# Performance work log

Hardware: AMD Instinct MI355X
Metric: run time of the kernel (lower is better)

The kernel has to match this reference:

```python
import jax, jax.numpy as jnp
import numpy as np

KAPPA = 0.5


def setup_inputs() -> dict:
    key = jax.random.key(0)
    embeddings = jax.random.normal(key, (8, 4096, 64), dtype=jnp.float32)
    return {"embeddings": embeddings}


def reference(embeddings):
    # logits[b, n, m] = kappa * <emb[b,n], emb[b,m]>   -> [B, N, N]
    logits = KAPPA * jnp.einsum("bnd,bmd->bnm", embeddings, embeddings)
    B = logits.shape[0]
    # logsumexp over both matrix dims, per batch element
    loss = jax.scipy.special.logsumexp(logits.reshape(B, -1), axis=1)
    return loss.mean()
```

## Files before the change

kernel.cpp:

```cpp
#include <hip/hip_runtime.h>
#include <math.h>

#define BATCH 8
#define NTOK  4096
#define DIM   64
#define BM    128
#define NT    (NTOK / BM)
#define TPB   (NT * (NT + 1) / 2)
#define TOTAL (BATCH * TPB)
#define GRIDP 1024
#define KAPPA 0.5f
#define LOG2E 1.4426950408889634f
#define LN2   0.6931471805599453f
#define M2FIX 48.0f

typedef _Float16 f16x8 __attribute__((ext_vector_type(8)));
typedef float    f32x16 __attribute__((ext_vector_type(16)));

__device__ __forceinline__ float EXP2(float x) {
#if __has_builtin(__builtin_amdgcn_exp2f)
    return __builtin_amdgcn_exp2f(x);
#else
    return __expf(x * LN2);
#endif
}

__global__ __launch_bounds__(256)
void conv_f16(const float* __restrict__ emb, f16x8* __restrict__ o16) {
    const size_t i = (size_t)blockIdx.x * 256 + threadIdx.x;
    const float4 v0 = *(const float4*)(emb + i * 8);
    const float4 v1 = *(const float4*)(emb + i * 8 + 4);
    f16x8 p;
    p[0] = (_Float16)v0.x; p[1] = (_Float16)v0.y;
    p[2] = (_Float16)v0.z; p[3] = (_Float16)v0.w;
    p[4] = (_Float16)v1.x; p[5] = (_Float16)v1.y;
    p[6] = (_Float16)v1.z; p[7] = (_Float16)v1.w;
    o16[i] = p;
}

__device__ __forceinline__ void decode_unit(int u, int& b, int& ti, int& tj) {
    b = u / TPB;
    int t = u - b * TPB;
    int i = 0;
    while (t >= NT - i) { t -= NT - i; ++i; }
    ti = i; tj = i + t;
}

__global__ __launch_bounds__(256, 4)
void gram_lse_partial(const f16x8* __restrict__ w16, float* __restrict__ ws) {
    __shared__ f16x8 S[2048];

    const int tid  = threadIdx.x;
    const int lane = tid & 63;
    const int w    = tid >> 6;
    const int half = lane >> 5;
    const int ln31 = lane & 31;
    const int waveR = (w & 1) * 64;
    const int waveC = (w >> 1) * 64;
    const float c2 = KAPPA * LOG2E;

    auto stage = [&](int b, int ti, int tj) {
        const char* pA16 = (const char*)(w16 + ((size_t)b * NTOK + (size_t)ti * BM) * 8);
        const char* pB16 = (const char*)(w16 + ((size_t)b * NTOK + (size_t)tj * BM) * 8);
        const char* pbase  = (w < 2) ? pA16 : pB16;
        const int   upBase = (w & 1) * 512 + lane;
#pragma unroll
        for (int q = 0; q < 8; ++q) {
            const int up  = upBase + q * 64;
            const int g   = up >> 7;
            const int rp  = up & 127;
            const int off = (((rp ^ g) << 7) | (g << 4));
            __builtin_amdgcn_global_load_lds(
                (const __attribute__((address_space(1))) void*)(pbase + off),
                (__attribute__((address_space(3))) void*)&S[(size_t)w * 512 + q * 64],
                16, 0, 0);
        }
    };

    int u = blockIdx.x;
    int b, ti, tj;
    decode_unit(u, b, ti, tj);
    stage(b, ti, tj);

    for (;;) {
        const float wgt = (ti == tj) ? 1.f : 2.f;
        const int   uc  = u;
        __syncthreads();

        f32x16 acc00 = {}, acc01 = {}, acc10 = {}, acc11 = {};
#pragma unroll
        for (int s = 0; s < 4; ++s) {
            const int g = 2 * s + half;
            const f16x8 a0 = S[g * BM + ((waveR + ln31) ^ g)];
            const f16x8 a1 = S[g * BM + ((waveR + 32 + ln31) ^ g)];
            const f16x8 b0 = S[1024 + g * BM + ((waveC + ln31) ^ g)];
            const f16x8 b1 = S[1024 + g * BM + ((waveC + 32 + ln31) ^ g)];
            acc00 = __builtin_amdgcn_mfma_f32_32x32x16_f16(a0, b0, acc00, 0, 0, 0);
            acc01 = __builtin_amdgcn_mfma_f32_32x32x16_f16(a0, b1, acc01, 0, 0, 0);
            acc10 = __builtin_amdgcn_mfma_f32_32x32x16_f16(a1, b0, acc10, 0, 0, 0);
            acc11 = __builtin_amdgcn_mfma_f32_32x32x16_f16(a1, b1, acc11, 0, 0, 0);
        }
        __syncthreads();

        u += GRIDP;
        const bool more = (u < TOTAL);
        if (more) {
            decode_unit(u, b, ti, tj);
            stage(b, ti, tj);
        }

        float s0 = 0.f, s1 = 0.f, s2 = 0.f, s3 = 0.f;
#pragma unroll
        for (int e = 0; e < 16; ++e) {
            s0 += EXP2(fmaf(c2, acc00[e], -M2FIX));
            s1 += EXP2(fmaf(c2, acc01[e], -M2FIX));
            s2 += EXP2(fmaf(c2, acc10[e], -M2FIX));
            s3 += EXP2(fmaf(c2, acc11[e], -M2FIX));
        }
        float lsum = (s0 + s1) + (s2 + s3);
#pragma unroll
        for (int off = 32; off > 0; off >>= 1)
            lsum += __shfl_xor(lsum, off);
        if (lane == 0) ws[4 * (size_t)uc + w] = wgt * lsum;

        if (!more) break;
    }
}

__global__ __launch_bounds__(512)
void reduce_lse(const float* __restrict__ ws, float* __restrict__ out) {
    const int tid  = threadIdx.x;
    const int w    = tid >> 6;
    const int lane = tid & 63;
    __shared__ float lse8[BATCH];

    const float* p = ws + (size_t)w * TPB * 4;
    float s = 0.f;
#pragma unroll
    for (int c = 0; c < 33; ++c) s += p[lane + 64 * c];
#pragma unroll
    for (int off = 32; off > 0; off >>= 1) s += __shfl_xor(s, off);

    if (lane == 0) lse8[w] = LN2 * (M2FIX + log2f(s));
    __syncthreads();
    if (tid == 0) {
        float a = 0.f;
        for (int i = 0; i < BATCH; ++i) a += lse8[i];
        out[0] = a * (1.f / BATCH);
    }
}

extern "C" void kernel_launch(void* const* d_in, const int* in_sizes, int n_in,
                              void* d_out, int out_size, void* d_ws, size_t ws_size,
                              hipStream_t stream) {
    const float* emb = (const float*)d_in[0];
    float* out = (float*)d_out;
    f16x8* w16 = (f16x8*)d_ws;
    float* prt = (float*)((char*)d_ws + (4u << 20));

    conv_f16<<<NTOK * BATCH * DIM / 8 / 256, 256, 0, stream>>>(emb, w16);
    gram_lse_partial<<<GRIDP, 256, 0, stream>>>(w16, prt);
    reduce_lse<<<1, 512, 0, stream>>>(prt, out);
}
```

Measured before the change: 83.97 us.

## Load MFMA operands directly from global memory and launch one block per tile

Drops the LDS staging buffer and the persistent-grid loop with its double-buffered global_load_lds prefetch. Each block now handles one tile pair and each wave reads its MFMA fragments straight from global memory into registers. The grid grows to the full tile count, and the occupancy hint falls from 4 to 3 blocks per CU. This removes barriers and LDS traffic, but each wave now loads its own fragments, so operand data is fetched several times per block with less reuse. It also loses the overlap between loading the next tile and running the exp reduction on the current one.

```diff
diff --git a/kernel.cpp b/kernel.cpp
--- a/kernel.cpp
+++ b/kernel.cpp
@@ -8,7 +8,6 @@
 #define NT    (NTOK / BM)
 #define TPB   (NT * (NT + 1) / 2)
 #define TOTAL (BATCH * TPB)
-#define GRIDP 1024
 #define KAPPA 0.5f
 #define LOG2E 1.4426950408889634f
 #define LN2   0.6931471805599453f
@@ -38,18 +37,8 @@
     o16[i] = p;
 }
 
-__device__ __forceinline__ void decode_unit(int u, int& b, int& ti, int& tj) {
-    b = u / TPB;
-    int t = u - b * TPB;
-    int i = 0;
-    while (t >= NT - i) { t -= NT - i; ++i; }
-    ti = i; tj = i + t;
-}
-
-__global__ __launch_bounds__(256, 4)
+__global__ __launch_bounds__(256, 3)
 void gram_lse_partial(const f16x8* __restrict__ w16, float* __restrict__ ws) {
-    __shared__ f16x8 S[2048];
-
     const int tid  = threadIdx.x;
     const int lane = tid & 63;
     const int w    = tid >> 6;
@@ -59,71 +48,54 @@
     const int waveC = (w >> 1) * 64;
     const float c2 = KAPPA * LOG2E;
 
-    auto stage = [&](int b, int ti, int tj) {
-        const char* pA16 = (const char*)(w16 + ((size_t)b * NTOK + (size_t)ti * BM) * 8);
-        const char* pB16 = (const char*)(w16 + ((size_t)b * NTOK + (size_t)tj * BM) * 8);
-        const char* pbase  = (w < 2) ? pA16 : pB16;
-        const int   upBase = (w & 1) * 512 + lane;
+    const int bb = blockIdx.x;
+    const int b  = bb / TPB;
+    int t = bb - b * TPB;
+    int ti = 0;
+    while (t >= NT - ti) { t -= NT - ti; ++ti; }
+    const int tj = ti + t;
+
+    const f16x8* pA = w16 + ((size_t)b * NTOK + (size_t)ti * BM) * 8;
+    const f16x8* pB = w16 + ((size_t)b * NTOK + (size_t)tj * BM) * 8;
+
+    const int rA0 = waveR + ln31, rA1 = rA0 + 32;
+    const int rB0 = waveC + ln31, rB1 = rB0 + 32;
+
+    f16x8 a0[4], a1[4], b0[4], b1[4];
 #pragma unroll
-        for (int q = 0; q < 8; ++q) {
-            const int up  = upBase + q * 64;
-            const int g   = up >> 7;
-            const int rp  = up & 127;
-            const int off = (((rp ^ g) << 7) | (g << 4));
-            __builtin_amdgcn_global_load_lds(
-                (const __attribute__((address_space(1))) void*)(pbase + off),
-                (__attribute__((address_space(3))) void*)&S[(size_t)w * 512 + q * 64],
-                16, 0, 0);
-        }
-    };
+    for (int s = 0; s < 4; ++s) {
+        const int g = 2 * s + half;
+        a0[s] = pA[rA0 * 8 + g];
+        a1[s] = pA[rA1 * 8 + g];
+        b0[s] = pB[rB0 * 8 + g];
+        b1[s] = pB[rB1 * 8 + g];
+    }
 
-    int u = blockIdx.x;
-    int b, ti, tj;
-    decode_unit(u, b, ti, tj);
-    stage(b, ti, tj);
+    f32x16 acc00 = {}, acc01 = {}, acc10 = {}, acc11 = {};
+#pragma unroll
+    for (int s = 0; s < 4; ++s) {
+        acc00 = __builtin_amdgcn_mfma_f32_32x32x16_f16(a0[s], b0[s], acc00, 0, 0, 0);
+        acc01 = __builtin_amdgcn_mfma_f32_32x32x16_f16(a0[s], b1[s], acc01, 0, 0, 0);
+        acc10 = __builtin_amdgcn_mfma_f32_32x32x16_f16(a1[s], b0[s], acc10, 0, 0, 0);
+        acc11 = __builtin_amdgcn_mfma_f32_32x32x16_f16(a1[s], b1[s], acc11, 0, 0, 0);
+    }
 
-    for (;;) {
+    float s0 = 0.f, s1 = 0.f, s2 = 0.f, s3 = 0.f;
+#pragma unroll
+    for (int e = 0; e < 16; ++e) {
+        s0 += EXP2(fmaf(c2, acc00[e], -M2FIX));
+        s1 += EXP2(fmaf(c2, acc01[e], -M2FIX));
+        s2 += EXP2(fmaf(c2, acc10[e], -M2FIX));
+        s3 += EXP2(fmaf(c2, acc11[e], -M2FIX));
+    }
+    float lsum = (s0 + s1) + (s2 + s3);
+#pragma unroll
+    for (int off = 32; off > 0; off >>= 1)
+        lsum += __shfl_xor(lsum, off);
+
+    if (lane == 0) {
         const float wgt = (ti == tj) ? 1.f : 2.f;
-        const int   uc  = u;
-        __syncthreads();
-
-        f32x16 acc00 = {}, acc01 = {}, acc10 = {}, acc11 = {};
-#pragma unroll
-        for (int s = 0; s < 4; ++s) {
-            const int g = 2 * s + half;
-            const f16x8 a0 = S[g * BM + ((waveR + ln31) ^ g)];
-            const f16x8 a1 = S[g * BM + ((waveR + 32 + ln31) ^ g)];
-            const f16x8 b0 = S[1024 + g * BM + ((waveC + ln31) ^ g)];
-            const f16x8 b1 = S[1024 + g * BM + ((waveC + 32 + ln31) ^ g)];
-            acc00 = __builtin_amdgcn_mfma_f32_32x32x16_f16(a0, b0, acc00, 0, 0, 0);
-            acc01 = __builtin_amdgcn_mfma_f32_32x32x16_f16(a0, b1, acc01, 0, 0, 0);
-            acc10 = __builtin_amdgcn_mfma_f32_32x32x16_f16(a1, b0, acc10, 0, 0, 0);
-            acc11 = __builtin_amdgcn_mfma_f32_32x32x16_f16(a1, b1, acc11, 0, 0, 0);
-        }
-        __syncthreads();
-
-        u += GRIDP;
-        const bool more = (u < TOTAL);
-        if (more) {
-            decode_unit(u, b, ti, tj);
-            stage(b, ti, tj);
-        }
-
-        float s0 = 0.f, s1 = 0.f, s2 = 0.f, s3 = 0.f;
-#pragma unroll
-        for (int e = 0; e < 16; ++e) {
-            s0 += EXP2(fmaf(c2, acc00[e], -M2FIX));
-            s1 += EXP2(fmaf(c2, acc01[e], -M2FIX));
-            s2 += EXP2(fmaf(c2, acc10[e], -M2FIX));
-            s3 += EXP2(fmaf(c2, acc11[e], -M2FIX));
-        }
-        float lsum = (s0 + s1) + (s2 + s3);
-#pragma unroll
-        for (int off = 32; off > 0; off >>= 1)
-            lsum += __shfl_xor(lsum, off);
-        if (lane == 0) ws[4 * (size_t)uc + w] = wgt * lsum;
-
-        if (!more) break;
+        ws[4 * (size_t)bb + w] = wgt * lsum;
     }
 }
 
@@ -159,6 +131,6 @@
     float* prt = (float*)((char*)d_ws + (4u << 20));
 
     conv_f16<<<NTOK * BATCH * DIM / 8 / 256, 256, 0, stream>>>(emb, w16);
-    gram_lse_partial<<<GRIDP, 256, 0, stream>>>(w16, prt);
+    gram_lse_partial<<<TOTAL, 256, 0, stream>>>(w16, prt);
     reduce_lse<<<1, 512, 0, stream>>>(prt, out);
 }
```

Result: slower. 92.66 us (+10.4%).

## Replace persistent prefetching loop with one block per tile and batch-interleaved ordering

Applied to the files above, without the earlier changes.

Drops the persistent grid of 1024 blocks that looped over tiles and prefetched the next tile into shared memory while finishing the current one's exponentials. Each block now handles a single 128x128 tile, and the grid covers all tiles (8*528). Block IDs are interleaved across batches so neighbouring blocks read from different batches. This removes the loop's bookkeeping and the serialising second barrier, relying on many resident blocks for overlap. In exchange it gives up explicit load/compute pipelining and adds per-block launch and staging overhead.

```diff
diff --git a/kernel.cpp b/kernel.cpp
--- a/kernel.cpp
+++ b/kernel.cpp
@@ -8,7 +8,6 @@
 #define NT    (NTOK / BM)
 #define TPB   (NT * (NT + 1) / 2)
 #define TOTAL (BATCH * TPB)
-#define GRIDP 1024
 #define KAPPA 0.5f
 #define LOG2E 1.4426950408889634f
 #define LN2   0.6931471805599453f
@@ -38,14 +37,6 @@
     o16[i] = p;
 }
 
-__device__ __forceinline__ void decode_unit(int u, int& b, int& ti, int& tj) {
-    b = u / TPB;
-    int t = u - b * TPB;
-    int i = 0;
-    while (t >= NT - i) { t -= NT - i; ++i; }
-    ti = i; tj = i + t;
-}
-
 __global__ __launch_bounds__(256, 4)
 void gram_lse_partial(const f16x8* __restrict__ w16, float* __restrict__ ws) {
     __shared__ f16x8 S[2048];
@@ -53,15 +44,18 @@
     const int tid  = threadIdx.x;
     const int lane = tid & 63;
     const int w    = tid >> 6;
-    const int half = lane >> 5;
-    const int ln31 = lane & 31;
-    const int waveR = (w & 1) * 64;
-    const int waveC = (w >> 1) * 64;
-    const float c2 = KAPPA * LOG2E;
+    const int p    = blockIdx.x;
+    const int bb   = (p & 7) * TPB + (p >> 3);
+    const int b    = bb / TPB;
+    int t = bb - b * TPB;
+    int ti = 0;
+    while (t >= NT - ti) { t -= NT - ti; ++ti; }
+    const int tj = ti + t;
 
-    auto stage = [&](int b, int ti, int tj) {
-        const char* pA16 = (const char*)(w16 + ((size_t)b * NTOK + (size_t)ti * BM) * 8);
-        const char* pB16 = (const char*)(w16 + ((size_t)b * NTOK + (size_t)tj * BM) * 8);
+    const char* pA16 = (const char*)(w16 + ((size_t)b * NTOK + (size_t)ti * BM) * 8);
+    const char* pB16 = (const char*)(w16 + ((size_t)b * NTOK + (size_t)tj * BM) * 8);
+
+    {
         const char* pbase  = (w < 2) ? pA16 : pB16;
         const int   upBase = (w & 1) * 512 + lane;
 #pragma unroll
@@ -75,55 +69,45 @@
                 (__attribute__((address_space(3))) void*)&S[(size_t)w * 512 + q * 64],
                 16, 0, 0);
         }
-    };
+    }
+    __syncthreads();
 
-    int u = blockIdx.x;
-    int b, ti, tj;
-    decode_unit(u, b, ti, tj);
-    stage(b, ti, tj);
+    const int half = lane >> 5;
+    const int ln31 = lane & 31;
+    const int waveR = (w & 1) * 64;
+    const int waveC = (w >> 1) * 64;
+    const float c2 = KAPPA * LOG2E;
 
-    for (;;) {
+    f32x16 acc00 = {}, acc01 = {}, acc10 = {}, acc11 = {};
+#pragma unroll
+    for (int s = 0; s < 4; ++s) {
+        const int g = 2 * s + half;
+        const f16x8 a0 = S[g * BM + ((waveR + ln31) ^ g)];
+        const f16x8 a1 = S[g * BM + ((waveR + 32 + ln31) ^ g)];
+        const f16x8 b0 = S[1024 + g * BM + ((waveC + ln31) ^ g)];
+        const f16x8 b1 = S[1024 + g * BM + ((waveC + 32 + ln31) ^ g)];
+        acc00 = __builtin_amdgcn_mfma_f32_32x32x16_f16(a0, b0, acc00, 0, 0, 0);
+        acc01 = __builtin_amdgcn_mfma_f32_32x32x16_f16(a0, b1, acc01, 0, 0, 0);
+        acc10 = __builtin_amdgcn_mfma_f32_32x32x16_f16(a1, b0, acc10, 0, 0, 0);
+        acc11 = __builtin_amdgcn_mfma_f32_32x32x16_f16(a1, b1, acc11, 0, 0, 0);
+    }
+
+    float s0 = 0.f, s1 = 0.f, s2 = 0.f, s3 = 0.f;
+#pragma unroll
+    for (int e = 0; e < 16; ++e) {
+        s0 += EXP2(fmaf(c2, acc00[e], -M2FIX));
+        s1 += EXP2(fmaf(c2, acc01[e], -M2FIX));
+        s2 += EXP2(fmaf(c2, acc10[e], -M2FIX));
+        s3 += EXP2(fmaf(c2, acc11[e], -M2FIX));
+    }
+    float lsum = (s0 + s1) + (s2 + s3);
+#pragma unroll
+    for (int off = 32; off > 0; off >>= 1)
+        lsum += __shfl_xor(lsum, off);
+
+    if (lane == 0) {
         const float wgt = (ti == tj) ? 1.f : 2.f;
-        const int   uc  = u;
-        __syncthreads();
-
-        f32x16 acc00 = {}, acc01 = {}, acc10 = {}, acc11 = {};
-#pragma unroll
-        for (int s = 0; s < 4; ++s) {
-            const int g = 2 * s + half;
-            const f16x8 a0 = S[g * BM + ((waveR + ln31) ^ g)];
-            const f16x8 a1 = S[g * BM + ((waveR + 32 + ln31) ^ g)];
-            const f16x8 b0 = S[1024 + g * BM + ((waveC + ln31) ^ g)];
-            const f16x8 b1 = S[1024 + g * BM + ((waveC + 32 + ln31) ^ g)];
-            acc00 = __builtin_amdgcn_mfma_f32_32x32x16_f16(a0, b0, acc00, 0, 0, 0);
-            acc01 = __builtin_amdgcn_mfma_f32_32x32x16_f16(a0, b1, acc01, 0, 0, 0);
-            acc10 = __builtin_amdgcn_mfma_f32_32x32x16_f16(a1, b0, acc10, 0, 0, 0);
-            acc11 = __builtin_amdgcn_mfma_f32_32x32x16_f16(a1, b1, acc11, 0, 0, 0);
-        }
-        __syncthreads();
-
-        u += GRIDP;
-        const bool more = (u < TOTAL);
-        if (more) {
-            decode_unit(u, b, ti, tj);
-            stage(b, ti, tj);
-        }
-
-        float s0 = 0.f, s1 = 0.f, s2 = 0.f, s3 = 0.f;
-#pragma unroll
-        for (int e = 0; e < 16; ++e) {
-            s0 += EXP2(fmaf(c2, acc00[e], -M2FIX));
-            s1 += EXP2(fmaf(c2, acc01[e], -M2FIX));
-            s2 += EXP2(fmaf(c2, acc10[e], -M2FIX));
-            s3 += EXP2(fmaf(c2, acc11[e], -M2FIX));
-        }
-        float lsum = (s0 + s1) + (s2 + s3);
-#pragma unroll
-        for (int off = 32; off > 0; off >>= 1)
-            lsum += __shfl_xor(lsum, off);
-        if (lane == 0) ws[4 * (size_t)uc + w] = wgt * lsum;
-
-        if (!more) break;
+        ws[4 * (size_t)bb + w] = wgt * lsum;
     }
 }
 
@@ -159,6 +143,6 @@
     float* prt = (float*)((char*)d_ws + (4u << 20));
 
     conv_f16<<<NTOK * BATCH * DIM / 8 / 256, 256, 0, stream>>>(emb, w16);
-    gram_lse_partial<<<GRIDP, 256, 0, stream>>>(w16, prt);
+    gram_lse_partial<<<TOTAL, 256, 0, stream>>>(w16, prt);
     reduce_lse<<<1, 512, 0, stream>>>(prt, out);
 }
```

Result: faster. 81.11 us (-3.4%).
